# Kernel optimization log

Measured on AMD Instinct MI355X. Metric: run time of the kernel, lower is better.

Reference implementation:

```python
import jax, jax.numpy as jnp
import numpy as np

B, ACT, C, H = 2048, 14, 128, 32
N = B * ACT                      # total nodes
E = B * ACT * ACT                # batched GCN edges
LOG_STD_MIN, LOG_STD_MAX = -20.0, 2.0


def setup_inputs() -> dict:
    key = jax.random.key(0)
    ks = jax.random.split(key, 8)
    def w(k, shape, fan_in):
        return jax.random.normal(k, shape, jnp.float32) / np.sqrt(fan_in).astype(np.float32)
    return {
        "state": jax.random.normal(ks[0], (N, C), jnp.float32),
        "conv_W": w(ks[1], (C, C), C),
        "conv_b": jnp.zeros((C,), jnp.float32),
        "lin1_W": w(ks[2], (2 * C, H), 2 * C),
        "lin1_b": jnp.zeros((H,), jnp.float32),
        "lin2_W": w(ks[3], (H, H), H),
        "lin2_b": jnp.zeros((H,), jnp.float32),
        "mu_W": w(ks[4], (H, 1), H),
        "mu_b": jnp.zeros((1,), jnp.float32),
        "sig_W": w(ks[5], (H, 1), H),
        "sig_b": jnp.zeros((1,), jnp.float32),
        "edge_index": jax.random.randint(ks[6], (2, E), 0, N, jnp.int32),
    }


def gcn_conv(x, W, b, src, dst):
    # PyG GCNConv default: add self-loops + symmetric normalization
    xw = x @ W                                           # [N, C]
    ones = jnp.ones(src.shape, x.dtype)
    deg = jax.ops.segment_sum(ones, dst, num_segments=N) + 1.0   # self-loop included
    dinv = jax.lax.rsqrt(deg)                            # deg^{-1/2}
    norm = dinv[src] * dinv[dst]                         # per-edge weight
    agg = jax.ops.segment_sum(xw[src] * norm[:, None], dst, num_segments=N)
    return agg + xw * (dinv * dinv)[:, None] + b         # self-loop term + bias


def reference(state, conv_W, conv_b, lin1_W, lin1_b, lin2_W, lin2_b,
              mu_W, mu_b, sig_W, sig_b, edge_index):
    src, dst = edge_index[0], edge_index[1]
    out = jax.nn.relu(gcn_conv(state, conv_W, conv_b, src, dst))
    x = (out + state).reshape(B, ACT, C)                 # [B, 14, C]
    # self.edges = all 196 directed pairs (i, j) over the 14-node graph
    e_src = jnp.repeat(jnp.arange(ACT), ACT)             # edges[:, 0]
    e_dst = jnp.tile(jnp.arange(ACT), ACT)               # edges[:, 1]
    ef = jnp.concatenate([x[:, e_src, :], x[:, e_dst, :]], axis=2)  # [B, 196, 2C]
    h = jax.nn.leaky_relu(ef @ lin1_W + lin1_b)          # slope 0.01 (torch default)
    h = jax.nn.leaky_relu(h @ lin2_W + lin2_b)           # [B, 196, H]
    log_std = jnp.clip(h @ sig_W + sig_b, LOG_STD_MIN, LOG_STD_MAX)
    std = jnp.exp(log_std)[..., 0]                       # [B, 196]
    mu = jax.nn.softplus(h @ mu_W + mu_b + 1e-10)[..., 0]  # [B, 196]
    # distribution parameters (return_D / deterministic paths)
    return jnp.stack([mu, std], axis=0)                  # [2, B, 196]
```

## Files before the change

### kernel.cpp

```cpp
#include <hip/hip_runtime.h>
#include <hip/hip_bf16.h>
#include <math.h>

#define NB    2048
#define ACT   14
#define NC    128
#define NH    32
#define NNODE (NB*ACT)
#define NEDGE (NB*ACT*ACT)
#define NPAIR (NB*ACT*ACT)
#define BCAP  64

typedef __attribute__((ext_vector_type(8))) short bf16x8;
typedef __attribute__((ext_vector_type(4))) float f32x4;

__device__ __forceinline__ unsigned short f2bf(float f)
{
    unsigned u = __float_as_uint(f);
    return (unsigned short)((u + 0x7fff + ((u >> 16) & 1)) >> 16);
}
__device__ __forceinline__ float bf2f(unsigned short h)
{
    return __uint_as_float(((unsigned)h) << 16);
}
__device__ __forceinline__ float bfl(unsigned v) { return __uint_as_float(v << 16); }
__device__ __forceinline__ float bfh(unsigned v) { return __uint_as_float(v & 0xffff0000u); }

__global__ __launch_bounds__(256) void init_misc(
    int* __restrict__ cnt, unsigned short* __restrict__ ydummy,
    const float* __restrict__ convW, unsigned short* __restrict__ convWt,
    const float* __restrict__ W1,
    unsigned short* __restrict__ Whi, unsigned short* __restrict__ Wlo,
    const float* __restrict__ W2, unsigned short* __restrict__ W2cm)
{
    int idx = blockIdx.x * 256 + threadIdx.x;
    if (idx < NNODE) cnt[idx] = 0;
    if (idx < 128) ydummy[idx] = 0;
    if (idx < 128 * 128) {
        int c = idx >> 7, k = idx & 127;
        convWt[idx] = f2bf(convW[k * 128 + c]);
    }
    if (idx < 64 * 128) {
        int c = idx >> 7, k = idx & 127;
        float w = (c < 32) ? W1[k * 32 + c] : W1[(128 + k) * 32 + (c - 32)];
        unsigned short h = f2bf(w);
        Whi[idx] = h;
        Wlo[idx] = f2bf(w - bf2f(h));
    }
    if (idx < 1024) {
        int c = idx >> 5, kk = idx & 31;
        W2cm[c * 32 + kk] = f2bf(W2[kk * 32 + c]);
    }
}

__global__ void bucket_fill(const int* __restrict__ src, const int* __restrict__ dst,
                            int* __restrict__ cnt, int* __restrict__ bucket)
{
    int e = blockIdx.x * blockDim.x + threadIdx.x;
    if (e < NEDGE) {
        int d = dst[e];
        int slot = atomicAdd(&cnt[d], 1);
        if (slot < BCAP) bucket[(size_t)d * BCAP + slot] = src[e];
    }
}

__global__ __launch_bounds__(256) void gemm1_mfma(
    const float* __restrict__ A, const unsigned short* __restrict__ Bt,
    const int* __restrict__ cnt, unsigned short* __restrict__ y)
{
    __shared__ unsigned short Ah[128 * 128];
    __shared__ unsigned short Alo[128 * 128];
    __shared__ unsigned short Bl[128 * 128];
    const int tid  = threadIdx.x;
    const int row0 = blockIdx.x * 128;

#pragma unroll
    for (int it = 0; it < 16; ++it) {
        int idx = tid + it * 256;
        int r = idx >> 5;
        int c = (idx & 31) << 2;
        float4 v = ((const float4*)(A + (size_t)(row0 + r) * 128))[idx & 31];
        ushort4 h, l;
        h.x = f2bf(v.x); l.x = f2bf(v.x - bf2f(h.x));
        h.y = f2bf(v.y); l.y = f2bf(v.y - bf2f(h.y));
        h.z = f2bf(v.z); l.z = f2bf(v.z - bf2f(h.z));
        h.w = f2bf(v.w); l.w = f2bf(v.w - bf2f(h.w));
        int byte = (r * 256 + c * 2) ^ ((r & 7) << 4);
        *(ushort4*)((char*)Ah  + byte) = h;
        *(ushort4*)((char*)Alo + byte) = l;
    }
#pragma unroll
    for (int it = 0; it < 8; ++it) {
        int idx = tid + it * 256;
        int cc = idx >> 4;
        int kk = (idx & 15) << 3;
        bf16x8 v = *((const bf16x8*)(Bt + cc * 128 + kk));
        int byte = (cc * 256 + kk * 2) ^ ((cc & 7) << 4);
        *(bf16x8*)((char*)Bl + byte) = v;
    }
    __syncthreads();

    const int wv = tid >> 6, lane = tid & 63;
    const int lr = lane & 15, kb = lane >> 4;
    const int col0 = wv * 32;

    f32x4 acc0[8], acc1[8];
#pragma unroll
    for (int mt = 0; mt < 8; ++mt) {
        acc0[mt] = (f32x4){0.f, 0.f, 0.f, 0.f};
        acc1[mt] = (f32x4){0.f, 0.f, 0.f, 0.f};
    }

#pragma unroll
    for (int ks = 0; ks < 4; ++ks) {
        const int kbyte = (ks * 32 + kb * 8) * 2;
        int cb0 = ((col0 + lr) * 256 + kbyte) ^ (((col0 + lr) & 7) << 4);
        int cb1 = ((col0 + 16 + lr) * 256 + kbyte) ^ (((col0 + 16 + lr) & 7) << 4);
        bf16x8 b0 = *(const bf16x8*)((char*)Bl + cb0);
        bf16x8 b1 = *(const bf16x8*)((char*)Bl + cb1);
#pragma unroll
        for (int mt = 0; mt < 8; ++mt) {
            int rr = mt * 16 + lr;
            int ab = (rr * 256 + kbyte) ^ ((rr & 7) << 4);
            bf16x8 ah = *(const bf16x8*)((char*)Ah  + ab);
            bf16x8 al = *(const bf16x8*)((char*)Alo + ab);
            acc0[mt] = __builtin_amdgcn_mfma_f32_16x16x32_bf16(ah, b0, acc0[mt], 0, 0, 0);
            acc0[mt] = __builtin_amdgcn_mfma_f32_16x16x32_bf16(al, b0, acc0[mt], 0, 0, 0);
            acc1[mt] = __builtin_amdgcn_mfma_f32_16x16x32_bf16(ah, b1, acc1[mt], 0, 0, 0);
            acc1[mt] = __builtin_amdgcn_mfma_f32_16x16x32_bf16(al, b1, acc1[mt], 0, 0, 0);
        }
    }

#pragma unroll
    for (int mt = 0; mt < 8; ++mt) {
#pragma unroll
        for (int t = 0; t < 4; ++t) {
            int grow = row0 + mt * 16 + kb * 4 + t;
            float s = rsqrtf((float)cnt[grow] + 1.0f);
            y[(size_t)grow * 128 + col0 + lr]      = f2bf(acc0[mt][t] * s);
            y[(size_t)grow * 128 + col0 + 16 + lr] = f2bf(acc1[mt][t] * s);
        }
    }
}

__global__ __launch_bounds__(256) void gemm2_mfma(
    const float* __restrict__ X, const unsigned short* __restrict__ Whi,
    const unsigned short* __restrict__ Wlo, float* __restrict__ U)
{
    __shared__ unsigned short Ah[64 * 128];
    __shared__ unsigned short Alo[64 * 128];
    __shared__ unsigned short Bh[64 * 128];
    __shared__ unsigned short Blo[64 * 128];
    const int tid  = threadIdx.x;
    const int row0 = blockIdx.x * 64;

#pragma unroll
    for (int it = 0; it < 8; ++it) {
        int idx = tid + it * 256;
        int r = idx >> 5;
        int c = (idx & 31) << 2;
        float4 v = ((const float4*)(X + (size_t)(row0 + r) * 128))[idx & 31];
        ushort4 h, l;
        h.x = f2bf(v.x); l.x = f2bf(v.x - bf2f(h.x));
        h.y = f2bf(v.y); l.y = f2bf(v.y - bf2f(h.y));
        h.z = f2bf(v.z); l.z = f2bf(v.z - bf2f(h.z));
        h.w = f2bf(v.w); l.w = f2bf(v.w - bf2f(h.w));
        int byte = (r * 256 + c * 2) ^ ((r & 7) << 4);
        *(ushort4*)((char*)Ah  + byte) = h;
        *(ushort4*)((char*)Alo + byte) = l;
    }
#pragma unroll
    for (int it = 0; it < 4; ++it) {
        int idx = tid + it * 256;
        int cc = idx >> 4;
        int kk = (idx & 15) << 3;
        int byte = (cc * 256 + kk * 2) ^ ((cc & 7) << 4);
        *(bf16x8*)((char*)Bh  + byte) = *((const bf16x8*)(Whi + cc * 128 + kk));
        *(bf16x8*)((char*)Blo + byte) = *((const bf16x8*)(Wlo + cc * 128 + kk));
    }
    __syncthreads();

    const int wv = tid >> 6, lane = tid & 63;
    const int lr = lane & 15, kb = lane >> 4;
    const int col0 = wv * 16;

    f32x4 acc[4];
#pragma unroll
    for (int mt = 0; mt < 4; ++mt) acc[mt] = (f32x4){0.f, 0.f, 0.f, 0.f};

#pragma unroll
    for (int ks = 0; ks < 4; ++ks) {
        const int kbyte = (ks * 32 + kb * 8) * 2;
        int cb = ((col0 + lr) * 256 + kbyte) ^ (((col0 + lr) & 7) << 4);
        bf16x8 bh = *(const bf16x8*)((char*)Bh  + cb);
        bf16x8 bl = *(const bf16x8*)((char*)Blo + cb);
#pragma unroll
        for (int mt = 0; mt < 4; ++mt) {
            int rr = mt * 16 + lr;
            int ab = (rr * 256 + kbyte) ^ ((rr & 7) << 4);
            bf16x8 ah = *(const bf16x8*)((char*)Ah  + ab);
            bf16x8 al = *(const bf16x8*)((char*)Alo + ab);
            acc[mt] = __builtin_amdgcn_mfma_f32_16x16x32_bf16(ah, bh, acc[mt], 0, 0, 0);
            acc[mt] = __builtin_amdgcn_mfma_f32_16x16x32_bf16(al, bh, acc[mt], 0, 0, 0);
            acc[mt] = __builtin_amdgcn_mfma_f32_16x16x32_bf16(ah, bl, acc[mt], 0, 0, 0);
        }
    }

#pragma unroll
    for (int mt = 0; mt < 4; ++mt) {
#pragma unroll
        for (int t = 0; t < 4; ++t) {
            int grow = row0 + mt * 16 + kb * 4 + t;
            U[(size_t)grow * 64 + col0 + lr] = acc[mt][t];
        }
    }
}

__global__ __launch_bounds__(256) void gather_agg(
    const int* __restrict__ bucket, const int* __restrict__ cnt,
    const unsigned short* __restrict__ y, const float* __restrict__ bias,
    const float* __restrict__ state, float* __restrict__ xout)
{
    const int lane = threadIdx.x & 31;
    const int d = (blockIdx.x * 256 + threadIdx.x) >> 5;
    if (d >= NNODE) return;

    const int c_true = cnt[d];
    const int c = c_true < BCAP ? c_true : BCAP;

    uint2 sv0 = ((const uint2*)(y + (size_t)d * NC))[lane];
    float4 acc;
    acc.x = bfl(sv0.x); acc.y = bfh(sv0.x);
    acc.z = bfl(sv0.y); acc.w = bfh(sv0.y);

    const int* brow = bucket + (size_t)d * BCAP;
    for (int base = 0; base < c; base += 32) {
        int rem = c - base;
        int m = rem < 32 ? rem : 32;
        int sv = (lane < m) ? brow[base + lane] : NNODE;
        int mm = (m + 3) & ~3;
        for (int j = 0; j < mm; j += 4) {
            int s0 = __shfl(sv, j + 0, 32);
            int s1 = __shfl(sv, j + 1, 32);
            int s2 = __shfl(sv, j + 2, 32);
            int s3 = __shfl(sv, j + 3, 32);
            uint2 a0 = ((const uint2*)(y + (size_t)s0 * NC))[lane];
            uint2 a1 = ((const uint2*)(y + (size_t)s1 * NC))[lane];
            uint2 a2 = ((const uint2*)(y + (size_t)s2 * NC))[lane];
            uint2 a3 = ((const uint2*)(y + (size_t)s3 * NC))[lane];
            acc.x += bfl(a0.x) + bfl(a1.x) + bfl(a2.x) + bfl(a3.x);
            acc.y += bfh(a0.x) + bfh(a1.x) + bfh(a2.x) + bfh(a3.x);
            acc.z += bfl(a0.y) + bfl(a1.y) + bfl(a2.y) + bfl(a3.y);
            acc.w += bfh(a0.y) + bfh(a1.y) + bfh(a2.y) + bfh(a3.y);
        }
    }

    const float dv = rsqrtf((float)c_true + 1.0f);
    float4 b  = ((const float4*)bias)[lane];
    float4 st = ((const float4*)(state + (size_t)d * NC))[lane];
    float4 r;
    r.x = fmaxf(acc.x * dv + b.x, 0.f) + st.x;
    r.y = fmaxf(acc.y * dv + b.y, 0.f) + st.y;
    r.z = fmaxf(acc.z * dv + b.z, 0.f) + st.z;
    r.w = fmaxf(acc.w * dv + b.w, 0.f) + st.w;
    ((float4*)(xout + (size_t)d * NC))[lane] = r;
}

__device__ __forceinline__ float softplusf(float z)
{
    return z > 0.f ? z + log1pf(expf(-z)) : log1pf(expf(z));
}
__device__ __forceinline__ float leakyf(float z)
{
    return z > 0.f ? z : 0.01f * z;
}

__global__ __launch_bounds__(256) void pairs_mfma5_kernel(
    const float* __restrict__ uv, const unsigned short* __restrict__ W2cm,
    const float* __restrict__ b1, const float* __restrict__ b2,
    const float* __restrict__ muW, const float* __restrict__ mu_b,
    const float* __restrict__ sigW, const float* __restrict__ sig_b,
    float* __restrict__ out)
{
    __shared__ float uvs[42 * 68];
    __shared__ float h2s[4][64 * 33];
    const int tid  = threadIdx.x;
    const int wv   = tid >> 6;
    const int lane = tid & 63;
    const int lr   = lane & 15;
    const int kb   = lane >> 4;
    const int k0   = kb * 8;
    const int b0 = (blockIdx.x * 256) / 196;
    const int nodebase = b0 * ACT;

#pragma unroll
    for (int it = 0; it < 3; ++it) {
        int c = tid + it * 256;
        if (c < 42 * 16) {
            int r = c >> 4, q = c & 15;
            if (nodebase + r < NNODE) {
                float4 v = ((const float4*)(uv + (size_t)(nodebase + r) * 64))[q];
                *((float4*)&uvs[r * 68 + q * 4]) = v;
            }
        }
    }
    bf16x8 bfr0 = *((const bf16x8*)(W2cm + (size_t)lr * 32 + k0));
    bf16x8 bfr1 = *((const bf16x8*)(W2cm + (size_t)(16 + lr) * 32 + k0));
    float4 c0 = *((const float4*)(b1 + k0));
    float4 c1 = *((const float4*)(b1 + k0 + 4));
    __syncthreads();

    float* h2w = h2s[wv];
#pragma unroll
    for (int tt = 0; tt < 4; ++tt) {
        const int g = blockIdx.x * 256 + wv * 64 + tt * 16 + lr;
        const int b = g / 196;
        const int p = g - b * 196;
        const int i = p / 14;
        const int j = p - i * 14;
        const float* up = &uvs[((b - b0) * ACT + i) * 68 + k0];
        const float* vp = &uvs[((b - b0) * ACT + j) * 68 + 32 + k0];
        float4 u0 = *((const float4*)up);
        float4 u1 = *((const float4*)(up + 4));
        float4 v0 = *((const float4*)vp);
        float4 v1 = *((const float4*)(vp + 4));

        bf16x8 a;
        a[0] = (short)f2bf(leakyf(u0.x + v0.x + c0.x));
        a[1] = (short)f2bf(leakyf(u0.y + v0.y + c0.y));
        a[2] = (short)f2bf(leakyf(u0.z + v0.z + c0.z));
        a[3] = (short)f2bf(leakyf(u0.w + v0.w + c0.w));
        a[4] = (short)f2bf(leakyf(u1.x + v1.x + c1.x));
        a[5] = (short)f2bf(leakyf(u1.y + v1.y + c1.y));
        a[6] = (short)f2bf(leakyf(u1.z + v1.z + c1.z));
        a[7] = (short)f2bf(leakyf(u1.w + v1.w + c1.w));

        f32x4 A0 = {0.f, 0.f, 0.f, 0.f};
        f32x4 A1 = {0.f, 0.f, 0.f, 0.f};
        A0 = __builtin_amdgcn_mfma_f32_16x16x32_bf16(a, bfr0, A0, 0, 0, 0);
        A1 = __builtin_amdgcn_mfma_f32_16x16x32_bf16(a, bfr1, A1, 0, 0, 0);

        const int rowb = tt * 16 + kb * 4;
#pragma unroll
        for (int t = 0; t < 4; ++t) {
            h2w[(rowb + t) * 33 + lr]      = A0[t];
            h2w[(rowb + t) * 33 + 16 + lr] = A1[t];
        }
    }

    float mu_acc = mu_b[0] + 1e-10f;
    float sg = sig_b[0];
    const float* myrow = &h2w[lane * 33];
#pragma unroll
    for (int l = 0; l < 32; ++l) {
        float h = myrow[l] + b2[l];
        h = h > 0.f ? h : 0.01f * h;
        mu_acc += h * muW[l];
        sg     += h * sigW[l];
    }
    const int g2 = blockIdx.x * 256 + wv * 64 + lane;
    out[g2]         = softplusf(mu_acc);
    out[NPAIR + g2] = expf(fminf(fmaxf(sg, -20.f), 2.f));
}

extern "C" void kernel_launch(void* const* d_in, const int* in_sizes, int n_in,
                              void* d_out, int out_size, void* d_ws, size_t ws_size,
                              hipStream_t stream)
{
    const float* state  = (const float*)d_in[0];
    const float* conv_W = (const float*)d_in[1];
    const float* conv_b = (const float*)d_in[2];
    const float* lin1_W = (const float*)d_in[3];
    const float* lin1_b = (const float*)d_in[4];
    const float* lin2_W = (const float*)d_in[5];
    const float* lin2_b = (const float*)d_in[6];
    const float* mu_W   = (const float*)d_in[7];
    const float* mu_b   = (const float*)d_in[8];
    const float* sig_W  = (const float*)d_in[9];
    const float* sig_b  = (const float*)d_in[10];
    const int*   eidx   = (const int*)d_in[11];
    const int* e_src = eidx;
    const int* e_dst = eidx + NEDGE;

    float* out = (float*)d_out;

    char* wsb = (char*)d_ws;
    unsigned short* y = (unsigned short*)wsb;
    char* p = wsb + (size_t)(NNODE + 1) * NC * sizeof(unsigned short);
    float* x = (float*)p;            p += (size_t)NNODE * NC * sizeof(float);
    int* cnt = (int*)p;              p += (size_t)NNODE * sizeof(int);
    int* bucket = (int*)p;           p += (size_t)NNODE * BCAP * sizeof(int);
    unsigned short* convWt = (unsigned short*)p;  p += 128 * 128 * sizeof(unsigned short);
    unsigned short* Whi = (unsigned short*)p;     p += 64 * 128 * sizeof(unsigned short);
    unsigned short* Wlo = (unsigned short*)p;     p += 64 * 128 * sizeof(unsigned short);
    unsigned short* W2cm = (unsigned short*)p;    p += 1024 * sizeof(unsigned short);
    float* uvb = (float*)p;

    init_misc<<<(NNODE + 255) / 256, 256, 0, stream>>>(
        cnt, y + (size_t)NNODE * NC, conv_W, convWt, lin1_W, Whi, Wlo,
        lin2_W, W2cm);

    bucket_fill<<<NEDGE / 256, 256, 0, stream>>>(e_src, e_dst, cnt, bucket);

    gemm1_mfma<<<NNODE / 128, 256, 0, stream>>>(state, convWt, cnt, y);

    gather_agg<<<(NNODE * 32) / 256, 256, 0, stream>>>(
        bucket, cnt, y, conv_b, state, x);

    gemm2_mfma<<<NNODE / 64, 256, 0, stream>>>(x, Whi, Wlo, uvb);

    pairs_mfma5_kernel<<<NPAIR / 256, 256, 0, stream>>>(
        uvb, W2cm, lin1_b, lin2_b, mu_W, mu_b, sig_W, sig_b, out);
}
```

Baseline: 76.93 us.

## Fuse neighbor gather-aggregation into the second GEMM kernel

```diff
diff --git a/kernel.cpp b/kernel.cpp
--- a/kernel.cpp
+++ b/kernel.cpp
@@ -143,9 +143,12 @@
     }
 }
 
-__global__ __launch_bounds__(256) void gemm2_mfma(
-    const float* __restrict__ X, const unsigned short* __restrict__ Whi,
-    const unsigned short* __restrict__ Wlo, float* __restrict__ U)
+__global__ __launch_bounds__(256) void gather_gemm2(
+    const int* __restrict__ bucket, const int* __restrict__ cnt,
+    const unsigned short* __restrict__ y, const float* __restrict__ bias,
+    const float* __restrict__ state,
+    const unsigned short* __restrict__ Whi, const unsigned short* __restrict__ Wlo,
+    float* __restrict__ U)
 {
     __shared__ unsigned short Ah[64 * 128];
     __shared__ unsigned short Alo[64 * 128];
@@ -153,22 +156,9 @@
     __shared__ unsigned short Blo[64 * 128];
     const int tid  = threadIdx.x;
     const int row0 = blockIdx.x * 64;
-
-#pragma unroll
-    for (int it = 0; it < 8; ++it) {
-        int idx = tid + it * 256;
-        int r = idx >> 5;
-        int c = (idx & 31) << 2;
-        float4 v = ((const float4*)(X + (size_t)(row0 + r) * 128))[idx & 31];
-        ushort4 h, l;
-        h.x = f2bf(v.x); l.x = f2bf(v.x - bf2f(h.x));
-        h.y = f2bf(v.y); l.y = f2bf(v.y - bf2f(h.y));
-        h.z = f2bf(v.z); l.z = f2bf(v.z - bf2f(h.z));
-        h.w = f2bf(v.w); l.w = f2bf(v.w - bf2f(h.w));
-        int byte = (r * 256 + c * 2) ^ ((r & 7) << 4);
-        *(ushort4*)((char*)Ah  + byte) = h;
-        *(ushort4*)((char*)Alo + byte) = l;
-    }
+    const int lane32 = tid & 31;
+    const int grp = tid >> 5;
+
 #pragma unroll
     for (int it = 0; it < 4; ++it) {
         int idx = tid + it * 256;
@@ -177,6 +167,59 @@
         int byte = (cc * 256 + kk * 2) ^ ((cc & 7) << 4);
         *(bf16x8*)((char*)Bh  + byte) = *((const bf16x8*)(Whi + cc * 128 + kk));
         *(bf16x8*)((char*)Blo + byte) = *((const bf16x8*)(Wlo + cc * 128 + kk));
+    }
+
+#pragma unroll
+    for (int sweep = 0; sweep < 8; ++sweep) {
+        const int r = sweep * 8 + grp;
+        const int d = row0 + r;
+
+        const int c_true = cnt[d];
+        const int c = c_true < BCAP ? c_true : BCAP;
+
+        uint2 sv0 = ((const uint2*)(y + (size_t)d * NC))[lane32];
+        float4 acc;
+        acc.x = bfl(sv0.x); acc.y = bfh(sv0.x);
+        acc.z = bfl(sv0.y); acc.w = bfh(sv0.y);
+
+        const int* brow = bucket + (size_t)d * BCAP;
+        for (int base = 0; base < c; base += 32) {
+            int rem = c - base;
+            int m = rem < 32 ? rem : 32;
+            int sv = (lane32 < m) ? brow[base + lane32] : NNODE;
+            int mm = (m + 3) & ~3;
+            for (int j = 0; j < mm; j += 4) {
+                int s0 = __shfl(sv, j + 0, 32);
+                int s1 = __shfl(sv, j + 1, 32);
+                int s2 = __shfl(sv, j + 2, 32);
+                int s3 = __shfl(sv, j + 3, 32);
+                uint2 a0 = ((const uint2*)(y + (size_t)s0 * NC))[lane32];
+                uint2 a1 = ((const uint2*)(y + (size_t)s1 * NC))[lane32];
+                uint2 a2 = ((const uint2*)(y + (size_t)s2 * NC))[lane32];
+                uint2 a3 = ((const uint2*)(y + (size_t)s3 * NC))[lane32];
+                acc.x += bfl(a0.x) + bfl(a1.x) + bfl(a2.x) + bfl(a3.x);
+                acc.y += bfh(a0.x) + bfh(a1.x) + bfh(a2.x) + bfh(a3.x);
+                acc.z += bfl(a0.y) + bfl(a1.y) + bfl(a2.y) + bfl(a3.y);
+                acc.w += bfh(a0.y) + bfh(a1.y) + bfh(a2.y) + bfh(a3.y);
+            }
+        }
+
+        const float dv = rsqrtf((float)c_true + 1.0f);
+        float4 b  = ((const float4*)bias)[lane32];
+        float4 st = ((const float4*)(state + (size_t)d * NC))[lane32];
+        float xr0 = fmaxf(acc.x * dv + b.x, 0.f) + st.x;
+        float xr1 = fmaxf(acc.y * dv + b.y, 0.f) + st.y;
+        float xr2 = fmaxf(acc.z * dv + b.z, 0.f) + st.z;
+        float xr3 = fmaxf(acc.w * dv + b.w, 0.f) + st.w;
+
+        ushort4 h, l;
+        h.x = f2bf(xr0); l.x = f2bf(xr0 - bf2f(h.x));
+        h.y = f2bf(xr1); l.y = f2bf(xr1 - bf2f(h.y));
+        h.z = f2bf(xr2); l.z = f2bf(xr2 - bf2f(h.z));
+        h.w = f2bf(xr3); l.w = f2bf(xr3 - bf2f(h.w));
+        int byte = (r * 256 + lane32 * 8) ^ ((r & 7) << 4);
+        *(ushort4*)((char*)Ah  + byte) = h;
+        *(ushort4*)((char*)Alo + byte) = l;
     }
     __syncthreads();
 
@@ -214,56 +257,6 @@
             U[(size_t)grow * 64 + col0 + lr] = acc[mt][t];
         }
     }
-}
-
-__global__ __launch_bounds__(256) void gather_agg(
-    const int* __restrict__ bucket, const int* __restrict__ cnt,
-    const unsigned short* __restrict__ y, const float* __restrict__ bias,
-    const float* __restrict__ state, float* __restrict__ xout)
-{
-    const int lane = threadIdx.x & 31;
-    const int d = (blockIdx.x * 256 + threadIdx.x) >> 5;
-    if (d >= NNODE) return;
-
-    const int c_true = cnt[d];
-    const int c = c_true < BCAP ? c_true : BCAP;
-
-    uint2 sv0 = ((const uint2*)(y + (size_t)d * NC))[lane];
-    float4 acc;
-    acc.x = bfl(sv0.x); acc.y = bfh(sv0.x);
-    acc.z = bfl(sv0.y); acc.w = bfh(sv0.y);
-
-    const int* brow = bucket + (size_t)d * BCAP;
-    for (int base = 0; base < c; base += 32) {
-        int rem = c - base;
-        int m = rem < 32 ? rem : 32;
-        int sv = (lane < m) ? brow[base + lane] : NNODE;
-        int mm = (m + 3) & ~3;
-        for (int j = 0; j < mm; j += 4) {
-            int s0 = __shfl(sv, j + 0, 32);
-            int s1 = __shfl(sv, j + 1, 32);
-            int s2 = __shfl(sv, j + 2, 32);
-            int s3 = __shfl(sv, j + 3, 32);
-            uint2 a0 = ((const uint2*)(y + (size_t)s0 * NC))[lane];
-            uint2 a1 = ((const uint2*)(y + (size_t)s1 * NC))[lane];
-            uint2 a2 = ((const uint2*)(y + (size_t)s2 * NC))[lane];
-            uint2 a3 = ((const uint2*)(y + (size_t)s3 * NC))[lane];
-            acc.x += bfl(a0.x) + bfl(a1.x) + bfl(a2.x) + bfl(a3.x);
-            acc.y += bfh(a0.x) + bfh(a1.x) + bfh(a2.x) + bfh(a3.x);
-            acc.z += bfl(a0.y) + bfl(a1.y) + bfl(a2.y) + bfl(a3.y);
-            acc.w += bfh(a0.y) + bfh(a1.y) + bfh(a2.y) + bfh(a3.y);
-        }
-    }
-
-    const float dv = rsqrtf((float)c_true + 1.0f);
-    float4 b  = ((const float4*)bias)[lane];
-    float4 st = ((const float4*)(state + (size_t)d * NC))[lane];
-    float4 r;
-    r.x = fmaxf(acc.x * dv + b.x, 0.f) + st.x;
-    r.y = fmaxf(acc.y * dv + b.y, 0.f) + st.y;
-    r.z = fmaxf(acc.z * dv + b.z, 0.f) + st.z;
-    r.w = fmaxf(acc.w * dv + b.w, 0.f) + st.w;
-    ((float4*)(xout + (size_t)d * NC))[lane] = r;
 }
 
 __device__ __forceinline__ float softplusf(float z)
@@ -387,7 +380,6 @@
     char* wsb = (char*)d_ws;
     unsigned short* y = (unsigned short*)wsb;
     char* p = wsb + (size_t)(NNODE + 1) * NC * sizeof(unsigned short);
-    float* x = (float*)p;            p += (size_t)NNODE * NC * sizeof(float);
     int* cnt = (int*)p;              p += (size_t)NNODE * sizeof(int);
     int* bucket = (int*)p;           p += (size_t)NNODE * BCAP * sizeof(int);
     unsigned short* convWt = (unsigned short*)p;  p += 128 * 128 * sizeof(unsigned short);
@@ -404,10 +396,8 @@
 
     gemm1_mfma<<<NNODE / 128, 256, 0, stream>>>(state, convWt, cnt, y);
 
-    gather_agg<<<(NNODE * 32) / 256, 256, 0, stream>>>(
-        bucket, cnt, y, conv_b, state, x);
-
-    gemm2_mfma<<<NNODE / 64, 256, 0, stream>>>(x, Whi, Wlo, uvb);
+    gather_gemm2<<<NNODE / 64, 256, 0, stream>>>(
+        bucket, cnt, y, conv_b, state, Whi, Wlo, uvb);
 
     pairs_mfma5_kernel<<<NPAIR / 256, 256, 0, stream>>>(
         uvb, W2cm, lin1_b, lin2_b, mu_W, mu_b, sig_W, sig_b, out);
```

Result: slower. 84.42 us (+9.7%).
